# Optimization experiments

Hardware: AMD Instinct MI355X
Metric: run time of the kernel (lower is better)

## Reference

```python
import jax, jax.numpy as jnp
from jax import lax
import numpy as np

B, V, S, K = 16, 8, 256, 66  # batch, predicates/example, seq len, num BIO tags


def setup_inputs() -> dict:
    key = jax.random.key(0)
    ks = jax.random.split(key, 9)
    return {
        "log_pa": jax.random.normal(ks[0], (B, S, S, K), jnp.float32),
        "score": jax.random.normal(ks[1], (B, S, S, K), jnp.float32),
        "v_label": jax.random.randint(ks[2], (B, V), 0, S, jnp.int32),
        "v_l": jnp.full((B,), V, jnp.int32),
        "orig_l": jax.random.randint(ks[3], (B,), S // 2, S + 1, jnp.int32),
        "role_label": jax.random.randint(ks[4], (B, V, S), 0, K, jnp.int32),
        "start_transitions": jax.random.normal(ks[5], (K,), jnp.float32),
        "transitions": jax.random.normal(ks[6], (K, K), jnp.float32),
        "end_transitions": jax.random.normal(ks[7], (K,), jnp.float32),
    }


def crf_log_likelihood(logits, tags, mask, start_t, trans, end_t):
    """allennlp ConditionalRandomField.forward: sum_n log p(tags_n | logits_n).
    logits [N,T,K] float, tags [N,T] int, mask [N,T] bool."""
    maskf = mask.astype(logits.dtype)

    # --- partition function via forward algorithm (sequential logsumexp scan) ---
    def alpha_step(alpha, x):
        logit_t, m_t = x  # [N,K], [N]
        # inner[n,i,j] = alpha[n,i] + trans[i,j] + logit_t[n,j]
        inner = alpha[:, :, None] + trans[None, :, :] + logit_t[:, None, :]
        new = jax.nn.logsumexp(inner, axis=1)  # [N,K]
        return jnp.where(m_t[:, None], new, alpha), None

    alpha0 = start_t[None, :] + logits[:, 0]  # [N,K]
    xs = (jnp.swapaxes(logits[:, 1:], 0, 1), jnp.swapaxes(mask[:, 1:], 0, 1))
    alpha, _ = lax.scan(alpha_step, alpha0, xs)
    log_z = jax.nn.logsumexp(alpha + end_t[None, :], axis=-1)  # [N]

    # --- joint score of gold path ---
    emit = jnp.take_along_axis(logits, tags[:, :, None].astype(jnp.int32), axis=2)[:, :, 0]  # [N,T]
    trans_sc = trans[tags[:, :-1], tags[:, 1:]]  # [N,T-1]
    score = start_t[tags[:, 0]]
    score = score + jnp.sum(emit[:, :-1] * maskf[:, :-1] + trans_sc * maskf[:, 1:], axis=1)
    last_idx = jnp.sum(mask.astype(jnp.int32), axis=1) - 1  # [N]
    last_tags = jnp.take_along_axis(tags, last_idx[:, None], axis=1)[:, 0]
    score = score + end_t[last_tags] + emit[:, -1] * maskf[:, -1]

    return jnp.sum(score - log_z)


def reference(log_pa, score, v_label, v_l, orig_l, role_label,
              start_transitions, transitions, end_transitions):
    # use_gold_predicate == 1 path of CRFLoss.forward, max_orig_l padded to S.
    # gather per-predicate score rows: a_score[b,k] = score[b, v_label[b,k]]
    a_score = score[jnp.arange(B)[:, None], v_label]          # [B,V,S,K]
    a_score = a_score.reshape(B * V, S, K)

    pos = jnp.arange(S)
    valid = pos[None, :] < orig_l[:, None]                    # [B,S] ragged length mask
    a_mask = jnp.broadcast_to(valid[:, None, :], (B, V, S)).reshape(B * V, S)
    a_gold = jnp.where(valid[:, None, :], role_label, 0).reshape(B * V, S)

    llh = crf_log_likelihood(a_score, a_gold, a_mask,
                             start_transitions, transitions, end_transitions)
    num_prop = B * V  # sum(v_l) with fixed V per example
    loss = llh / jnp.float32(num_prop)

    pred_idx = jnp.argmax(log_pa, axis=-1)  # [B,S,S] quick greedy decode
    return loss, pred_idx
```

## Files before the change

### kernel.cpp

```cpp
#include <hip/hip_runtime.h>
#include <cfloat>

#define Bdim 16
#define Vdim 8
#define Sdim 256
#define Kdim 66
#define NSEQ (Bdim * Vdim)
#define TPB 256
#define NROW (Bdim * Sdim * Sdim)
#define ARGMAX_BLOCKS (NROW / (2 * TPB))

__global__ __launch_bounds__(TPB) void crf_fused(
    const float* __restrict__ log_pa,
    const float* __restrict__ score,
    const int*   __restrict__ v_label,
    const int*   __restrict__ orig_l,
    const int*   __restrict__ role_label,
    const float* __restrict__ start_t,
    const float* __restrict__ trans,
    const float* __restrict__ end_t,
    float* __restrict__ out,
    float* __restrict__ ws)
{
  const int tid = threadIdx.x;
  const int bid = blockIdx.x;

  if (bid >= NSEQ) {
    const int gt = (bid - NSEQ) * TPB + tid;
    const float4* p4 = reinterpret_cast<const float4*>(log_pa) + (size_t)gt * 33;
    float best0 = -FLT_MAX, best1 = -FLT_MAX;
    int i0 = 0, i1 = 0;
#pragma unroll
    for (int q = 0; q < 33; ++q) {
      float4 w = p4[q];
      float v[4] = {w.x, w.y, w.z, w.w};
#pragma unroll
      for (int c = 0; c < 4; ++c) {
        int e = 4 * q + c;
        if (e < Kdim) {
          if (v[c] > best0) { best0 = v[c]; i0 = e; }
        } else {
          int e1 = e - Kdim;
          if (v[c] > best1) { best1 = v[c]; i1 = e1; }
        }
      }
    }
    float* o = out + 1 + (size_t)gt * 2;
    o[0] = (float)i0;
    o[1] = (float)i1;
    return;
  }

  __shared__ __align__(16) float sP[Kdim + 2];
  __shared__ float sRed[TPB];
  __shared__ int   sG[Sdim];
  __shared__ float sM;

  const int n  = bid;
  const int b  = n / Vdim;
  const int v  = n % Vdim;
  const int L  = orig_l[b];
  const int sl = v_label[b * Vdim + v];
  const float* logits = score + (size_t)(b * Sdim + sl) * Sdim * Kdim;

  sG[tid] = role_label[(size_t)n * Sdim + tid];

  float E[Kdim];
  float alpha = 0.f;
  if (tid < Kdim) {
#pragma unroll
    for (int i = 0; i < Kdim; ++i)
      E[i] = __expf(trans[i * Kdim + tid]);
    alpha = start_t[tid] + logits[tid];
  }
  __syncthreads();

  {
    const int t = tid;
    float c = 0.f;
    if (t < L) {
      int g = sG[t];
      c = logits[t * Kdim + g];
      if (t > 0) c += trans[sG[t - 1] * Kdim + g];
    }
    sRed[tid] = c;
  }
  __syncthreads();
  for (int off = TPB / 2; off > 0; off >>= 1) {
    if (tid < off) sRed[tid] += sRed[tid + off];
    __syncthreads();
  }
  float goldReg = 0.f;
  if (tid == 0)
    goldReg = sRed[0] + start_t[sG[0]] + end_t[sG[L - 1]];

  const float4* sP4 = reinterpret_cast<const float4*>(sP);
  for (int t = 1; t < L; ++t) {
    float lt = 0.f;
    if (tid < Kdim) lt = logits[t * Kdim + tid];
    if (tid == 0) sM = alpha;
    __syncthreads();
    const float m = sM;
    if (tid < Kdim) sP[tid] = __expf(alpha - m);
    __syncthreads();
    if (tid < Kdim) {
      float s0 = 0.f, s1 = 0.f, s2 = 0.f, s3 = 0.f;
#pragma unroll
      for (int q = 0; q < 16; ++q) {
        float4 p = sP4[q];
        s0 = fmaf(p.x, E[4 * q + 0], s0);
        s1 = fmaf(p.y, E[4 * q + 1], s1);
        s2 = fmaf(p.z, E[4 * q + 2], s2);
        s3 = fmaf(p.w, E[4 * q + 3], s3);
      }
      s0 = fmaf(sP[64], E[64], s0);
      s1 = fmaf(sP[65], E[65], s1);
      float s = (s0 + s1) + (s2 + s3);
      alpha = m + __logf(s) + lt;
    }
  }

  __syncthreads();
  if (tid < Kdim) sP[tid] = alpha + end_t[tid];
  __syncthreads();
  if (tid == 0) {
    float mm = -FLT_MAX;
    for (int i = 0; i < Kdim; ++i) mm = fmaxf(mm, sP[i]);
    float ss = 0.f;
    for (int i = 0; i < Kdim; ++i) ss += __expf(sP[i] - mm);
    float logz = mm + __logf(ss);
    ws[n] = goldReg - logz;
  }
}

__global__ void finalize_loss(const float* __restrict__ ws, float* __restrict__ out) {
  __shared__ float r[NSEQ];
  int tid = threadIdx.x;
  r[tid] = ws[tid];
  __syncthreads();
  for (int off = NSEQ / 2; off > 0; off >>= 1) {
    if (tid < off) r[tid] += r[tid + off];
    __syncthreads();
  }
  if (tid == 0) out[0] = r[0] / (float)NSEQ;
}

extern "C" void kernel_launch(void* const* d_in, const int* in_sizes, int n_in,
                              void* d_out, int out_size, void* d_ws, size_t ws_size,
                              hipStream_t stream) {
  const float* log_pa     = (const float*)d_in[0];
  const float* score      = (const float*)d_in[1];
  const int*   v_label    = (const int*)d_in[2];
  const int*   orig_l     = (const int*)d_in[4];
  const int*   role_label = (const int*)d_in[5];
  const float* start_t    = (const float*)d_in[6];
  const float* trans      = (const float*)d_in[7];
  const float* end_t      = (const float*)d_in[8];
  float* out = (float*)d_out;
  float* ws  = (float*)d_ws;

  dim3 grid(NSEQ + ARGMAX_BLOCKS);
  crf_fused<<<grid, TPB, 0, stream>>>(log_pa, score, v_label, orig_l, role_label,
                                      start_t, trans, end_t, out, ws);
  finalize_loss<<<1, NSEQ, 0, stream>>>(ws, out);
}
```

Baseline: 602.0 us.

## Run CRF forward recursion in one wave with staged LDS logits and argmax

The forward-algorithm loop now runs in a single 64-lane wavefront. Tags 64 and 65 are handled by lane 0 plus shuffle reductions, so each timestep needs only wave-level barriers instead of two block-wide __syncthreads. The other three waves compute the gold-path score and double-buffer the logits into LDS in 64-step chunks. The argmax path stages 128 rows per block through LDS with coalesced float4 loads, then runs one thread per row. The cost is extra serial work on lane 0 and shuffle reductions on every step.

```diff
diff --git a/kernel.cpp b/kernel.cpp
--- a/kernel.cpp
+++ b/kernel.cpp
@@ -5,10 +5,20 @@
 #define Vdim 8
 #define Sdim 256
 #define Kdim 66
-#define NSEQ (Bdim * Vdim)
+#define NSEQ 128
 #define TPB 256
 #define NROW (Bdim * Sdim * Sdim)
-#define ARGMAX_BLOCKS (NROW / (2 * TPB))
+#define ROWS_PER_BLK 128
+#define AMAX_BLOCKS (NROW / ROWS_PER_BLK)
+#define CHUNK 64
+#define CHUNK_F (CHUNK * Kdim)
+#define CHUNK_V4 (CHUNK_F / 4)
+
+__device__ __forceinline__ void lds_fence_wave() {
+  asm volatile("" ::: "memory");
+  __builtin_amdgcn_wave_barrier();
+  asm volatile("" ::: "memory");
+}
 
 __global__ __launch_bounds__(TPB) void crf_fused(
     const float* __restrict__ log_pa,
@@ -22,39 +32,35 @@
     float* __restrict__ out,
     float* __restrict__ ws)
 {
+  __shared__ __align__(16) float sBuf[2][CHUNK_F];
+  __shared__ __align__(16) float sP[68];
+  __shared__ float sGoldW[4];
+  __shared__ int   sG[Sdim];
+
   const int tid = threadIdx.x;
   const int bid = blockIdx.x;
 
   if (bid >= NSEQ) {
-    const int gt = (bid - NSEQ) * TPB + tid;
-    const float4* p4 = reinterpret_cast<const float4*>(log_pa) + (size_t)gt * 33;
-    float best0 = -FLT_MAX, best1 = -FLT_MAX;
-    int i0 = 0, i1 = 0;
-#pragma unroll
-    for (int q = 0; q < 33; ++q) {
-      float4 w = p4[q];
-      float v[4] = {w.x, w.y, w.z, w.w};
-#pragma unroll
-      for (int c = 0; c < 4; ++c) {
-        int e = 4 * q + c;
-        if (e < Kdim) {
-          if (v[c] > best0) { best0 = v[c]; i0 = e; }
-        } else {
-          int e1 = e - Kdim;
-          if (v[c] > best1) { best1 = v[c]; i1 = e1; }
-        }
-      }
-    }
-    float* o = out + 1 + (size_t)gt * 2;
-    o[0] = (float)i0;
-    o[1] = (float)i1;
+    const int ab = bid - NSEQ;
+    float* sA = &sBuf[0][0];
+    const float4* g4 = reinterpret_cast<const float4*>(log_pa + (size_t)ab * ROWS_PER_BLK * Kdim);
+    float4* s4 = reinterpret_cast<float4*>(sA);
+#pragma unroll
+    for (int f = tid; f < 2 * CHUNK_V4; f += TPB) s4[f] = g4[f];
+    __syncthreads();
+    if (tid < ROWS_PER_BLK) {
+      const float2* row2 = reinterpret_cast<const float2*>(sA + tid * Kdim);
+      float best = -FLT_MAX; int bi = 0;
+#pragma unroll
+      for (int q = 0; q < 33; ++q) {
+        float2 v = row2[q];
+        if (v.x > best) { best = v.x; bi = 2 * q; }
+        if (v.y > best) { best = v.y; bi = 2 * q + 1; }
+      }
+      out[1 + (size_t)ab * ROWS_PER_BLK + tid] = (float)bi;
+    }
     return;
   }
-
-  __shared__ __align__(16) float sP[Kdim + 2];
-  __shared__ float sRed[TPB];
-  __shared__ int   sG[Sdim];
-  __shared__ float sM;
 
   const int n  = bid;
   const int b  = n / Vdim;
@@ -63,73 +69,120 @@
   const int sl = v_label[b * Vdim + v];
   const float* logits = score + (size_t)(b * Sdim + sl) * Sdim * Kdim;
 
-  sG[tid] = role_label[(size_t)n * Sdim + tid];
-
-  float E[Kdim];
-  float alpha = 0.f;
-  if (tid < Kdim) {
-#pragma unroll
-    for (int i = 0; i < Kdim; ++i)
-      E[i] = __expf(trans[i * Kdim + tid]);
-    alpha = start_t[tid] + logits[tid];
+  {
+    float4* dst = reinterpret_cast<float4*>(sBuf[0]);
+    const float4* src = reinterpret_cast<const float4*>(logits);
+    for (int f = tid; f < CHUNK_V4; f += TPB) dst[f] = src[f];
+    sG[tid] = role_label[(size_t)n * Sdim + tid];
   }
   __syncthreads();
 
-  {
-    const int t = tid;
-    float c = 0.f;
-    if (t < L) {
-      int g = sG[t];
-      c = logits[t * Kdim + g];
-      if (t > 0) c += trans[sG[t - 1] * Kdim + g];
-    }
-    sRed[tid] = c;
-  }
-  __syncthreads();
-  for (int off = TPB / 2; off > 0; off >>= 1) {
-    if (tid < off) sRed[tid] += sRed[tid + off];
+  const int lane = tid;
+  float Ecol[Kdim];
+  float T64 = 0.f, T65 = 0.f, C44 = 0.f, C45 = 0.f, C54 = 0.f, C55 = 0.f;
+  float alphaA = 0.f, alpha64 = 0.f, alpha65 = 0.f;
+
+  if (tid < 64) {
+#pragma unroll
+    for (int i = 0; i < Kdim; ++i) Ecol[i] = __expf(trans[i * Kdim + lane]);
+    T64 = __expf(trans[lane * Kdim + 64]);
+    T65 = __expf(trans[lane * Kdim + 65]);
+    C44 = __expf(trans[64 * Kdim + 64]); C45 = __expf(trans[64 * Kdim + 65]);
+    C54 = __expf(trans[65 * Kdim + 64]); C55 = __expf(trans[65 * Kdim + 65]);
+    alphaA = start_t[lane] + sBuf[0][lane];
+    if (lane == 0) {
+      alpha64 = start_t[64] + sBuf[0][64];
+      alpha65 = start_t[65] + sBuf[0][65];
+    }
+  } else {
+    int idx = tid - 64;
+    float acc = 0.f;
+    for (int t = idx; t < Sdim; t += 192) {
+      if (t < L) {
+        int g = sG[t];
+        float e = logits[t * Kdim + g];
+        if (t > 0) e += trans[sG[t - 1] * Kdim + g];
+        acc += e;
+      }
+    }
+#pragma unroll
+    for (int off = 32; off > 0; off >>= 1) acc += __shfl_xor(acc, off, 64);
+    if ((tid & 63) == 0) sGoldW[tid >> 6] = acc;
+  }
+
+  for (int c = 0; c < 4; ++c) {
+    if (tid >= 64) {
+      if (c < 3) {
+        float4* dst = reinterpret_cast<float4*>(sBuf[(c + 1) & 1]);
+        const float4* src = reinterpret_cast<const float4*>(logits + (size_t)(c + 1) * CHUNK_F);
+        for (int f = tid - 64; f < CHUNK_V4; f += 192) dst[f] = src[f];
+      }
+    } else {
+      const float* bufc = sBuf[c & 1];
+      const int t0 = (c == 0) ? 1 : c * CHUNK;
+      const int t1 = min(L, (c + 1) * CHUNK);
+      const float4* sP4 = reinterpret_cast<const float4*>(sP);
+      for (int t = t0; t < t1; ++t) {
+        const float* rowp = bufc + (t - c * CHUNK) * Kdim;
+        float lt = rowp[lane];
+        float m  = __shfl(alphaA, 0, 64);
+        float pA = __expf(alphaA - m);
+        float p64 = 0.f, p65 = 0.f;
+        sP[lane] = pA;
+        if (lane == 0) {
+          p64 = __expf(alpha64 - m);
+          p65 = __expf(alpha65 - m);
+          sP[64] = p64; sP[65] = p65;
+        }
+        lds_fence_wave();
+        float s0 = 0.f, s1 = 0.f, s2 = 0.f, s3 = 0.f;
+#pragma unroll
+        for (int q = 0; q < 16; ++q) {
+          float4 p = sP4[q];
+          s0 = fmaf(p.x, Ecol[4 * q + 0], s0);
+          s1 = fmaf(p.y, Ecol[4 * q + 1], s1);
+          s2 = fmaf(p.z, Ecol[4 * q + 2], s2);
+          s3 = fmaf(p.w, Ecol[4 * q + 3], s3);
+        }
+        s0 = fmaf(sP[64], Ecol[64], s0);
+        s1 = fmaf(sP[65], Ecol[65], s1);
+        float dot = (s0 + s1) + (s2 + s3);
+        float s64 = pA * T64, s65 = pA * T65;
+#pragma unroll
+        for (int off = 32; off > 0; off >>= 1) {
+          s64 += __shfl_xor(s64, off, 64);
+          s65 += __shfl_xor(s65, off, 64);
+        }
+        alphaA = m + __logf(dot) + lt;
+        if (lane == 0) {
+          s64 += p64 * C44 + p65 * C54;
+          s65 += p64 * C45 + p65 * C55;
+          alpha64 = m + __logf(s64) + rowp[64];
+          alpha65 = m + __logf(s65) + rowp[65];
+        }
+        lds_fence_wave();
+      }
+    }
     __syncthreads();
   }
-  float goldReg = 0.f;
-  if (tid == 0)
-    goldReg = sRed[0] + start_t[sG[0]] + end_t[sG[L - 1]];
-
-  const float4* sP4 = reinterpret_cast<const float4*>(sP);
-  for (int t = 1; t < L; ++t) {
-    float lt = 0.f;
-    if (tid < Kdim) lt = logits[t * Kdim + tid];
-    if (tid == 0) sM = alpha;
-    __syncthreads();
-    const float m = sM;
-    if (tid < Kdim) sP[tid] = __expf(alpha - m);
-    __syncthreads();
-    if (tid < Kdim) {
-      float s0 = 0.f, s1 = 0.f, s2 = 0.f, s3 = 0.f;
-#pragma unroll
-      for (int q = 0; q < 16; ++q) {
-        float4 p = sP4[q];
-        s0 = fmaf(p.x, E[4 * q + 0], s0);
-        s1 = fmaf(p.y, E[4 * q + 1], s1);
-        s2 = fmaf(p.z, E[4 * q + 2], s2);
-        s3 = fmaf(p.w, E[4 * q + 3], s3);
-      }
-      s0 = fmaf(sP[64], E[64], s0);
-      s1 = fmaf(sP[65], E[65], s1);
-      float s = (s0 + s1) + (s2 + s3);
-      alpha = m + __logf(s) + lt;
-    }
-  }
-
-  __syncthreads();
-  if (tid < Kdim) sP[tid] = alpha + end_t[tid];
-  __syncthreads();
-  if (tid == 0) {
-    float mm = -FLT_MAX;
-    for (int i = 0; i < Kdim; ++i) mm = fmaxf(mm, sP[i]);
-    float ss = 0.f;
-    for (int i = 0; i < Kdim; ++i) ss += __expf(sP[i] - mm);
-    float logz = mm + __logf(ss);
-    ws[n] = goldReg - logz;
+
+  if (tid < 64) {
+    sP[lane] = alphaA + end_t[lane];
+    if (lane == 0) {
+      sP[64] = alpha64 + end_t[64];
+      sP[65] = alpha65 + end_t[65];
+    }
+    lds_fence_wave();
+    if (lane == 0) {
+      float M = -FLT_MAX;
+      for (int i = 0; i < Kdim; ++i) M = fmaxf(M, sP[i]);
+      float S = 0.f;
+      for (int i = 0; i < Kdim; ++i) S += __expf(sP[i] - M);
+      float logz = M + __logf(S);
+      float gold = sGoldW[1] + sGoldW[2] + sGoldW[3]
+                 + start_t[sG[0]] + end_t[sG[L - 1]];
+      ws[n] = gold - logz;
+    }
   }
 }
 
@@ -159,7 +212,7 @@
   float* out = (float*)d_out;
   float* ws  = (float*)d_ws;
 
-  dim3 grid(NSEQ + ARGMAX_BLOCKS);
+  dim3 grid(NSEQ + AMAX_BLOCKS);
   crf_fused<<<grid, TPB, 0, stream>>>(log_pa, score, v_label, orig_l, role_label,
                                       start_t, trans, end_t, out, ws);
   finalize_loss<<<1, NSEQ, 0, stream>>>(ws, out);
```

Measured after the change: 533.3 us. 11.4% less time.
